# Kernel optimization log

Hardware: AMD Instinct MI355X
Metric: run time of the kernel (lower is better)

## Reference

```python
import jax, jax.numpy as jnp
from jax import lax
import numpy as np

B, T, I, H, C = 32, 256, 128, 128, 100


def setup_inputs() -> dict:
    key = jax.random.key(0)
    ks = jax.random.split(key, 9)
    s = 1.0 / np.sqrt(H)  # PyTorch LSTMCell init range
    inp = {
        "x": jax.random.normal(ks[0], (B, T, I), dtype=jnp.float32),
        "w_ih": jax.random.uniform(ks[1], (4 * H, I), jnp.float32, -s, s),
        "b_ih": jax.random.uniform(ks[2], (4 * H,), jnp.float32, -s, s),
        "w_hh": jax.random.uniform(ks[3], (4 * H, H), jnp.float32, -s, s),
        "b_hh": jax.random.uniform(ks[4], (4 * H,), jnp.float32, -s, s),
        # attention params: normal(mean=0, std=0.01) per the source
        "w1": 0.01 * jax.random.normal(ks[5], (2 * H, H), dtype=jnp.float32),
        "w2": 0.01 * jax.random.normal(ks[6], (H, 1), dtype=jnp.float32),
        "w_fc": jax.random.uniform(ks[7], (C, H), jnp.float32, -s, s),
        "b_fc": jax.random.uniform(ks[8], (C,), jnp.float32, -s, s),
    }
    return inp


def _forward(x, w_ih, b_ih, w_hh, b_hh, w1, w2, w_fc, b_fc):
    Bv, Tv, _ = x.shape
    Hv = w_hh.shape[1]
    h0 = jnp.zeros((Bv, Hv), x.dtype)
    c0 = jnp.zeros((Bv, Hv), x.dtype)
    # memory buffer: slot 0 holds the initial zero hidden state (as in the
    # torch code, h_old starts as h_t=0); slots 1..T filled as we go.
    # Unwritten (future) slots are zero, so their attn contribution
    # attn_w * h_old is exactly zero -> no mask needed, matching the
    # growing-memory semantics of the original loop.
    mem0 = jnp.zeros((Bv, Tv + 1, Hv), x.dtype)
    attn0 = jnp.zeros((Bv, Hv), x.dtype)

    def step(carry, inp):
        h, c, mem, _ = carry
        x_t, i = inp
        # PyTorch LSTMCell: gate order i, f, g, o
        gates = x_t @ w_ih.T + b_ih + h @ w_hh.T + b_hh
        ig, fg, gg, og = jnp.split(gates, 4, axis=-1)
        c = jax.nn.sigmoid(fg) * c + jax.nn.sigmoid(ig) * jnp.tanh(gg)
        h = jax.nn.sigmoid(og) * jnp.tanh(c)
        # additive attention scores over the memory (NO softmax in source)
        h_rep = jnp.broadcast_to(h[:, None, :], mem.shape)  # [B, T+1, H]
        cat = jnp.concatenate([h_rep, mem], axis=-1)        # [B, T+1, 2H]
        s = jnp.tanh(cat @ w1) @ w2                          # [B, T+1, 1]
        attn_c = jnp.sum(s * mem, axis=1)                    # [B, H]
        mem = mem.at[:, i + 1, :].set(h)  # append h_t to memory
        return (h, c, mem, attn_c), None

    xs = (jnp.transpose(x, (1, 0, 2)), jnp.arange(Tv))
    (h, c, mem, attn_c), _ = lax.scan(step, (h0, c0, mem0, attn0), xs)
    return (h + attn_c) @ w_fc.T + b_fc


def reference(x, w_ih, b_ih, w_hh, b_hh, w1, w2, w_fc, b_fc):
    return _forward(x, w_ih, b_ih, w_hh, b_hh, w1, w2, w_fc, b_fc)
```

## Files before the change

### kernel.cpp

```cpp
#include <hip/hip_runtime.h>
#include <hip/hip_bf16.h>


#define Bsz 32
#define Tsz 256
#define Isz 128
#define Hsz 128
#define Csz 100
#define G4H 512

__device__ __forceinline__ float2 pk_fma(float2 a, float2 b, float2 c) {
    float2 d;
    asm("v_pk_fma_f32 %0, %1, %2, %3" : "=v"(d) : "v"(a), "v"(b), "v"(c));
    return d;
}
__device__ __forceinline__ float quad_rsum(float x) {
    int t = __builtin_amdgcn_update_dpp(0, __float_as_int(x), 0xB1, 0xF, 0xF, true);
    x += __int_as_float(t);
    t = __builtin_amdgcn_update_dpp(0, __float_as_int(x), 0x4E, 0xF, 0xF, true);
    x += __int_as_float(t);
    return x;
}
__device__ __forceinline__ float rcpf(float x) { return __builtin_amdgcn_rcpf(x); }
__device__ __forceinline__ float sigm_n(float x) { return rcpf(1.0f + __expf(-x)); }
__device__ __forceinline__ float tanh_n(float x) {
    float ax = fabsf(x);
    float e = __expf(-2.0f * ax);
    float t = (1.0f - e) * rcpf(1.0f + e);
    return copysignf(t, x);
}
__device__ __forceinline__ float sigm(float x) { return rcpf(1.0f + __expf(-x)); }
__device__ __forceinline__ float tanh_s(float x) {
    float ax = fabsf(x);
    float e = __expf(-2.0f * ax);
    float t = (1.0f - e) * rcpf(1.0f + e);
    return copysignf(t, x);
}

__global__ __launch_bounds__(256) void prep_kernel(
    const float* __restrict__ w_ih, const float* __restrict__ b_ih,
    const float* __restrict__ w_hh, const float* __restrict__ b_hh,
    float* __restrict__ wih_t, float* __restrict__ whh_pk, float* __restrict__ bias) {
    int idx = blockIdx.x * blockDim.x + threadIdx.x;
    if (idx < G4H * Isz) {
        int j = idx >> 7;
        int k = idx & 127;
        wih_t[k * G4H + j] = w_ih[idx];

        int j4  = idx & 3;
        int q   = (idx >> 2) & 3;
        int d   = (idx >> 4) & 127;
        int gi  = (idx >> 11) & 3;
        int kk4 = (idx >> 13) & 7;
        whh_pk[idx] = w_hh[(size_t)((gi << 7) + d) * 128 + (q << 5) + (kk4 << 2) + j4];
    }
    if (idx < G4H) bias[idx] = b_ih[idx] + b_hh[idx];
}

#define BM 64
#define BN 64
#define BKt 64
#define LDP 68

__global__ __launch_bounds__(256) void gemm_tn(
    const float* __restrict__ A, const float* __restrict__ Bm,
    const float* __restrict__ bias, float* __restrict__ C,
    int M, int N, int K) {
    __shared__ float As[BKt][LDP];
    __shared__ float Bs[BKt][LDP];
    int tid = threadIdx.x;
    int bm = blockIdx.y * BM;
    int bn = blockIdx.x * BN;
    int tx = tid & 15, ty = tid >> 4;
    float acc[4][4] = {};

    int lr = tid >> 4;
    int lc = (tid & 15) * 4;

    for (int k0 = 0; k0 < K; k0 += BKt) {
        #pragma unroll
        for (int p = 0; p < 4; ++p) {
            int row = p * 16 + lr;
            float4 v = *(const float4*)(A + (size_t)(bm + row) * K + k0 + lc);
            As[lc + 0][row] = v.x;
            As[lc + 1][row] = v.y;
            As[lc + 2][row] = v.z;
            As[lc + 3][row] = v.w;
        }
        #pragma unroll
        for (int p = 0; p < 4; ++p) {
            int kr = p * 16 + lr;
            float4 v = *(const float4*)(Bm + (size_t)(k0 + kr) * N + bn + lc);
            *(float4*)&Bs[kr][lc] = v;
        }
        __syncthreads();
        #pragma unroll
        for (int kk = 0; kk < BKt; ++kk) {
            float4 a = *(const float4*)&As[kk][ty * 4];
            float4 b = *(const float4*)&Bs[kk][tx * 4];
            acc[0][0] = fmaf(a.x, b.x, acc[0][0]);
            acc[0][1] = fmaf(a.x, b.y, acc[0][1]);
            acc[0][2] = fmaf(a.x, b.z, acc[0][2]);
            acc[0][3] = fmaf(a.x, b.w, acc[0][3]);
            acc[1][0] = fmaf(a.y, b.x, acc[1][0]);
            acc[1][1] = fmaf(a.y, b.y, acc[1][1]);
            acc[1][2] = fmaf(a.y, b.z, acc[1][2]);
            acc[1][3] = fmaf(a.y, b.w, acc[1][3]);
            acc[2][0] = fmaf(a.z, b.x, acc[2][0]);
            acc[2][1] = fmaf(a.z, b.y, acc[2][1]);
            acc[2][2] = fmaf(a.z, b.z, acc[2][2]);
            acc[2][3] = fmaf(a.z, b.w, acc[2][3]);
            acc[3][0] = fmaf(a.w, b.x, acc[3][0]);
            acc[3][1] = fmaf(a.w, b.y, acc[3][1]);
            acc[3][2] = fmaf(a.w, b.z, acc[3][2]);
            acc[3][3] = fmaf(a.w, b.w, acc[3][3]);
        }
        __syncthreads();
    }
    float bb[4] = {0.f, 0.f, 0.f, 0.f};
    if (bias) {
        bb[0] = bias[bn + tx * 4 + 0];
        bb[1] = bias[bn + tx * 4 + 1];
        bb[2] = bias[bn + tx * 4 + 2];
        bb[3] = bias[bn + tx * 4 + 3];
    }
    #pragma unroll
    for (int i = 0; i < 4; ++i) {
        int row = bm + ty * 4 + i;
        float4 v;
        v.x = acc[i][0] + bb[0];
        v.y = acc[i][1] + bb[1];
        v.z = acc[i][2] + bb[2];
        v.w = acc[i][3] + bb[3];
        *(float4*)(C + (size_t)row * N + bn + tx * 4) = v;
    }
}

#define HPAD(k) ((k) + 8 * ((k) >> 5))

__global__ __launch_bounds__(512, 2) void lstm_seq(
    const float* __restrict__ G, const float* __restrict__ whh_pk,
    float* __restrict__ H_all) {
    const int b = blockIdx.x;
    const int tid = threadIdx.x;
    const int d = tid >> 2;
    const int q = tid & 3;

    __shared__ float h_s[2][160];

    float2 w2[4][16];
    {
        const float4* wp = (const float4*)whh_pk;
        #pragma unroll
        for (int kk4 = 0; kk4 < 8; ++kk4)
            #pragma unroll
            for (int gi = 0; gi < 4; ++gi) {
                float4 v = wp[((kk4 * 4 + gi) * 128 + d) * 4 + q];
                w2[gi][kk4 * 2]     = make_float2(v.x, v.y);
                w2[gi][kk4 * 2 + 1] = make_float2(v.z, v.w);
            }
    }

    if (tid < 320) ((float*)h_s)[tid] = 0.0f;
    float c = 0.0f;
    __syncthreads();

    const float* Gq = G + (size_t)b * Tsz * G4H + q * 128 + d;
    float* Hb = H_all + (size_t)b * Tsz * Hsz + d;

    float gval = Gq[0];
    int cur = 0;
    for (int t = 0; t < Tsz; ++t) {
        const int tn = (t < Tsz - 1) ? t + 1 : t;
        float ngval = Gq[(size_t)tn * G4H];

        float2 acc0 = make_float2(q == 0 ? gval : 0.f, 0.f);
        float2 acc1 = make_float2(q == 1 ? gval : 0.f, 0.f);
        float2 acc2 = make_float2(q == 2 ? gval : 0.f, 0.f);
        float2 acc3 = make_float2(q == 3 ? gval : 0.f, 0.f);
        const float4* hb4 = (const float4*)&h_s[cur][q * 40];
        #pragma unroll
        for (int kk4 = 0; kk4 < 8; ++kk4) {
            float4 h4 = hb4[kk4];
            float2 hA = make_float2(h4.x, h4.y);
            float2 hB = make_float2(h4.z, h4.w);
            acc0 = pk_fma(hA, w2[0][2 * kk4], acc0);
            acc1 = pk_fma(hA, w2[1][2 * kk4], acc1);
            acc2 = pk_fma(hA, w2[2][2 * kk4], acc2);
            acc3 = pk_fma(hA, w2[3][2 * kk4], acc3);
            acc0 = pk_fma(hB, w2[0][2 * kk4 + 1], acc0);
            acc1 = pk_fma(hB, w2[1][2 * kk4 + 1], acc1);
            acc2 = pk_fma(hB, w2[2][2 * kk4 + 1], acc2);
            acc3 = pk_fma(hB, w2[3][2 * kk4 + 1], acc3);
        }
        float a0 = quad_rsum(acc0.x + acc0.y);
        float a1 = quad_rsum(acc1.x + acc1.y);
        float a2 = quad_rsum(acc2.x + acc2.y);
        float a3 = quad_rsum(acc3.x + acc3.y);

        float iv = sigm_n(a0);
        float fv = sigm_n(a1);
        float gv = tanh_n(a2);
        float ov = sigm_n(a3);
        c = fv * c + iv * gv;
        float h = ov * tanh_n(c);

        int nxt = cur ^ 1;
        if (q == 0) {
            h_s[nxt][HPAD(d)] = h;
            Hb[(size_t)t * Hsz] = h;
        }
        gval = ngval;
        __syncthreads();
        cur = nxt;
    }
}

__global__ __launch_bounds__(256) void attn_out(
    const float* __restrict__ H_all, const float* __restrict__ KV,
    const float* __restrict__ w1, const float* __restrict__ w2,
    const float* __restrict__ w_fc, const float* __restrict__ b_fc,
    float* __restrict__ out) {
    int b = blockIdx.x;
    int tid = threadIdx.x;
    __shared__ float hT[Hsz];
    __shared__ float q_s[Hsz];
    __shared__ float s_s[Tsz];
    __shared__ float r_s[Hsz];

    const float* Hb = H_all + (size_t)b * Tsz * Hsz;
    const float* KVb = KV + (size_t)b * Tsz * Hsz;

    if (tid < Hsz) hT[tid] = Hb[255 * Hsz + tid];
    __syncthreads();
    if (tid < Hsz) {
        float acc = 0.f;
        #pragma unroll 8
        for (int k = 0; k < Hsz; ++k) acc = fmaf(hT[k], w1[k * Hsz + tid], acc);
        q_s[tid] = acc;
    }
    __syncthreads();
    int wave = tid >> 6, lane = tid & 63;
    float w2a = w2[lane], w2b = w2[lane + 64];
    for (int j = wave; j < 255; j += 4) {
        const float* kv = KVb + j * Hsz;
        float v0 = q_s[lane] + kv[lane];
        float v1 = q_s[lane + 64] + kv[lane + 64];
        float p = tanh_s(v0) * w2a + tanh_s(v1) * w2b;
        #pragma unroll
        for (int off = 32; off > 0; off >>= 1) p += __shfl_xor(p, off);
        if (lane == 0) s_s[j] = p;
    }
    __syncthreads();
    if (tid < Hsz) {
        float acc = 0.f;
        #pragma unroll 4
        for (int j = 0; j < 255; ++j) acc = fmaf(s_s[j], Hb[j * Hsz + tid], acc);
        r_s[tid] = hT[tid] + acc;
    }
    __syncthreads();
    if (tid < Csz) {
        float acc = b_fc[tid];
        const float* wr = w_fc + tid * Hsz;
        #pragma unroll 8
        for (int k = 0; k < Hsz; ++k) acc = fmaf(r_s[k], wr[k], acc);
        out[b * Csz + tid] = acc;
    }
}

extern "C" void kernel_launch(void* const* d_in, const int* in_sizes, int n_in,
                              void* d_out, int out_size, void* d_ws, size_t ws_size,
                              hipStream_t stream) {
    const float* x    = (const float*)d_in[0];
    const float* w_ih = (const float*)d_in[1];
    const float* b_ih = (const float*)d_in[2];
    const float* w_hh = (const float*)d_in[3];
    const float* b_hh = (const float*)d_in[4];
    const float* w1   = (const float*)d_in[5];
    const float* w2   = (const float*)d_in[6];
    const float* w_fc = (const float*)d_in[7];
    const float* b_fc = (const float*)d_in[8];

    float* ws = (float*)d_ws;
    float* wih_t  = ws;
    float* whh_pk = wih_t + 65536;
    float* bias   = whh_pk + 65536;
    float* G      = bias + 512;
    float* H_all  = G + 4194304;
    float* KV     = H_all + 1048576;

    prep_kernel<<<256, 256, 0, stream>>>(w_ih, b_ih, w_hh, b_hh, wih_t, whh_pk, bias);

    dim3 g1(G4H / BN, (Bsz * Tsz) / BM);
    gemm_tn<<<g1, 256, 0, stream>>>(x, wih_t, bias, G, Bsz * Tsz, G4H, Isz);

    lstm_seq<<<Bsz, 512, 0, stream>>>(G, whh_pk, H_all);

    dim3 g2(Hsz / BN, (Bsz * Tsz) / BM);
    gemm_tn<<<g2, 256, 0, stream>>>(H_all, w1 + Hsz * Hsz, nullptr, KV, Bsz * Tsz, Hsz, Hsz);

    attn_out<<<Bsz, 256, 0, stream>>>(H_all, KV, w1, w2, w_fc, b_fc, (float*)d_out);
}
```

Measured before the change: 355.5 us.

## Use 128x128 GEMM tiles, batch H stores via ring, and reparallelize attention

```diff
diff --git a/kernel.cpp b/kernel.cpp
--- a/kernel.cpp
+++ b/kernel.cpp
@@ -29,13 +29,7 @@
     float t = (1.0f - e) * rcpf(1.0f + e);
     return copysignf(t, x);
 }
-__device__ __forceinline__ float sigm(float x) { return rcpf(1.0f + __expf(-x)); }
-__device__ __forceinline__ float tanh_s(float x) {
-    float ax = fabsf(x);
-    float e = __expf(-2.0f * ax);
-    float t = (1.0f - e) * rcpf(1.0f + e);
-    return copysignf(t, x);
-}
+__device__ __forceinline__ float tanh_s(float x) { return tanh_n(x); }
 
 __global__ __launch_bounds__(256) void prep_kernel(
     const float* __restrict__ w_ih, const float* __restrict__ b_ih,
@@ -55,6 +49,74 @@
         whh_pk[idx] = w_hh[(size_t)((gi << 7) + d) * 128 + (q << 5) + (kk4 << 2) + j4];
     }
     if (idx < G4H) bias[idx] = b_ih[idx] + b_hh[idx];
+}
+
+#define GBK 16
+#define GLD 132
+
+__global__ __launch_bounds__(256) void gemm128(
+    const float* __restrict__ A, const float* __restrict__ Bm,
+    const float* __restrict__ bias, float* __restrict__ C,
+    int M, int N, int K) {
+    __shared__ float As[GBK][GLD];
+    __shared__ float Bs[GBK][GLD];
+    const int tid = threadIdx.x;
+    const int bm = blockIdx.y * 128;
+    const int bn = blockIdx.x * 128;
+    const int tx = tid & 15, ty = tid >> 4;
+    float acc[8][8] = {};
+
+    const int ar = tid >> 2;
+    const int ac = (tid & 3) * 4;
+    const int br = tid >> 5;
+    const int bc = (tid & 31) * 4;
+
+    for (int k0 = 0; k0 < K; k0 += GBK) {
+        #pragma unroll
+        for (int h = 0; h < 2; ++h) {
+            int r = ar + 64 * h;
+            float4 v = *(const float4*)(A + (size_t)(bm + r) * K + k0 + ac);
+            As[ac + 0][r] = v.x;
+            As[ac + 1][r] = v.y;
+            As[ac + 2][r] = v.z;
+            As[ac + 3][r] = v.w;
+        }
+        #pragma unroll
+        for (int h = 0; h < 2; ++h) {
+            int kr = br + 8 * h;
+            float4 v = *(const float4*)(Bm + (size_t)(k0 + kr) * N + bn + bc);
+            *(float4*)&Bs[kr][bc] = v;
+        }
+        __syncthreads();
+        #pragma unroll
+        for (int kk = 0; kk < GBK; ++kk) {
+            float a[8], b[8];
+            *(float4*)&a[0] = *(const float4*)&As[kk][ty * 8];
+            *(float4*)&a[4] = *(const float4*)&As[kk][ty * 8 + 4];
+            *(float4*)&b[0] = *(const float4*)&Bs[kk][tx * 8];
+            *(float4*)&b[4] = *(const float4*)&Bs[kk][tx * 8 + 4];
+            #pragma unroll
+            for (int i = 0; i < 8; ++i)
+                #pragma unroll
+                for (int j = 0; j < 8; ++j)
+                    acc[i][j] = fmaf(a[i], b[j], acc[i][j]);
+        }
+        __syncthreads();
+    }
+    float bb[8];
+    #pragma unroll
+    for (int j = 0; j < 8; ++j) bb[j] = bias ? bias[bn + tx * 8 + j] : 0.0f;
+    #pragma unroll
+    for (int i = 0; i < 8; ++i) {
+        int row = bm + ty * 8 + i;
+        float4 v0, v1;
+        v0.x = acc[i][0] + bb[0]; v0.y = acc[i][1] + bb[1];
+        v0.z = acc[i][2] + bb[2]; v0.w = acc[i][3] + bb[3];
+        v1.x = acc[i][4] + bb[4]; v1.y = acc[i][5] + bb[5];
+        v1.z = acc[i][6] + bb[6]; v1.w = acc[i][7] + bb[7];
+        *(float4*)(C + (size_t)row * N + bn + tx * 8) = v0;
+        *(float4*)(C + (size_t)row * N + bn + tx * 8 + 4) = v1;
+    }
 }
 
 #define BM 64
@@ -147,8 +209,9 @@
     const int q = tid & 3;
 
     __shared__ float h_s[2][160];
-
-    float2 w2[4][16];
+    __shared__ float ring[8][Hsz];
+
+    float2 w2v[4][16];
     {
         const float4* wp = (const float4*)whh_pk;
         #pragma unroll
@@ -156,8 +219,8 @@
             #pragma unroll
             for (int gi = 0; gi < 4; ++gi) {
                 float4 v = wp[((kk4 * 4 + gi) * 128 + d) * 4 + q];
-                w2[gi][kk4 * 2]     = make_float2(v.x, v.y);
-                w2[gi][kk4 * 2 + 1] = make_float2(v.z, v.w);
+                w2v[gi][kk4 * 2]     = make_float2(v.x, v.y);
+                w2v[gi][kk4 * 2 + 1] = make_float2(v.z, v.w);
             }
     }
 
@@ -166,7 +229,10 @@
     __syncthreads();
 
     const float* Gq = G + (size_t)b * Tsz * G4H + q * 128 + d;
-    float* Hb = H_all + (size_t)b * Tsz * Hsz + d;
+    float* Hb = H_all + (size_t)b * Tsz * Hsz;
+
+    const int fr = tid >> 6;
+    const int fc = (tid * 2) & 127;
 
     float gval = Gq[0];
     int cur = 0;
@@ -174,29 +240,31 @@
         const int tn = (t < Tsz - 1) ? t + 1 : t;
         float ngval = Gq[(size_t)tn * G4H];
 
-        float2 acc0 = make_float2(q == 0 ? gval : 0.f, 0.f);
-        float2 acc1 = make_float2(q == 1 ? gval : 0.f, 0.f);
-        float2 acc2 = make_float2(q == 2 ? gval : 0.f, 0.f);
-        float2 acc3 = make_float2(q == 3 ? gval : 0.f, 0.f);
+        float2 accA[4], accB[4];
+        #pragma unroll
+        for (int gi = 0; gi < 4; ++gi) {
+            accA[gi] = make_float2(q == gi ? gval : 0.f, 0.f);
+            accB[gi] = make_float2(0.f, 0.f);
+        }
         const float4* hb4 = (const float4*)&h_s[cur][q * 40];
         #pragma unroll
         for (int kk4 = 0; kk4 < 8; ++kk4) {
             float4 h4 = hb4[kk4];
             float2 hA = make_float2(h4.x, h4.y);
             float2 hB = make_float2(h4.z, h4.w);
-            acc0 = pk_fma(hA, w2[0][2 * kk4], acc0);
-            acc1 = pk_fma(hA, w2[1][2 * kk4], acc1);
-            acc2 = pk_fma(hA, w2[2][2 * kk4], acc2);
-            acc3 = pk_fma(hA, w2[3][2 * kk4], acc3);
-            acc0 = pk_fma(hB, w2[0][2 * kk4 + 1], acc0);
-            acc1 = pk_fma(hB, w2[1][2 * kk4 + 1], acc1);
-            acc2 = pk_fma(hB, w2[2][2 * kk4 + 1], acc2);
-            acc3 = pk_fma(hB, w2[3][2 * kk4 + 1], acc3);
-        }
-        float a0 = quad_rsum(acc0.x + acc0.y);
-        float a1 = quad_rsum(acc1.x + acc1.y);
-        float a2 = quad_rsum(acc2.x + acc2.y);
-        float a3 = quad_rsum(acc3.x + acc3.y);
+            accA[0] = pk_fma(hA, w2v[0][2 * kk4], accA[0]);
+            accA[1] = pk_fma(hA, w2v[1][2 * kk4], accA[1]);
+            accA[2] = pk_fma(hA, w2v[2][2 * kk4], accA[2]);
+            accA[3] = pk_fma(hA, w2v[3][2 * kk4], accA[3]);
+            accB[0] = pk_fma(hB, w2v[0][2 * kk4 + 1], accB[0]);
+            accB[1] = pk_fma(hB, w2v[1][2 * kk4 + 1], accB[1]);
+            accB[2] = pk_fma(hB, w2v[2][2 * kk4 + 1], accB[2]);
+            accB[3] = pk_fma(hB, w2v[3][2 * kk4 + 1], accB[3]);
+        }
+        float a0 = quad_rsum(accA[0].x + accA[0].y + accB[0].x + accB[0].y);
+        float a1 = quad_rsum(accA[1].x + accA[1].y + accB[1].x + accB[1].y);
+        float a2 = quad_rsum(accA[2].x + accA[2].y + accB[2].x + accB[2].y);
+        float a3 = quad_rsum(accA[3].x + accA[3].y + accB[3].x + accB[3].y);
 
         float iv = sigm_n(a0);
         float fv = sigm_n(a1);
@@ -208,11 +276,16 @@
         int nxt = cur ^ 1;
         if (q == 0) {
             h_s[nxt][HPAD(d)] = h;
-            Hb[(size_t)t * Hsz] = h;
+            ring[t & 7][d] = h;
         }
         gval = ngval;
         __syncthreads();
         cur = nxt;
+
+        if ((t & 7) == 7) {
+            float2 v = *(const float2*)&ring[fr][fc];
+            *(float2*)&Hb[(size_t)(t - 7 + fr) * Hsz + fc] = v;
+        }
     }
 }
 
@@ -225,13 +298,18 @@
     int tid = threadIdx.x;
     __shared__ float hT[Hsz];
     __shared__ float q_s[Hsz];
+    __shared__ float w2s[Hsz];
     __shared__ float s_s[Tsz];
+    __shared__ float r2[2][Hsz];
     __shared__ float r_s[Hsz];
 
     const float* Hb = H_all + (size_t)b * Tsz * Hsz;
     const float* KVb = KV + (size_t)b * Tsz * Hsz;
 
-    if (tid < Hsz) hT[tid] = Hb[255 * Hsz + tid];
+    if (tid < Hsz) {
+        hT[tid] = Hb[255 * Hsz + tid];
+        w2s[tid] = w2[tid];
+    }
     __syncthreads();
     if (tid < Hsz) {
         float acc = 0.f;
@@ -240,31 +318,48 @@
         q_s[tid] = acc;
     }
     __syncthreads();
-    int wave = tid >> 6, lane = tid & 63;
-    float w2a = w2[lane], w2b = w2[lane + 64];
-    for (int j = wave; j < 255; j += 4) {
-        const float* kv = KVb + j * Hsz;
-        float v0 = q_s[lane] + kv[lane];
-        float v1 = q_s[lane + 64] + kv[lane + 64];
-        float p = tanh_s(v0) * w2a + tanh_s(v1) * w2b;
-        #pragma unroll
-        for (int off = 32; off > 0; off >>= 1) p += __shfl_xor(p, off);
-        if (lane == 0) s_s[j] = p;
-    }
-    __syncthreads();
-    if (tid < Hsz) {
+
+    const int qd = tid >> 2, ql = tid & 3;
+    #pragma unroll
+    for (int jj = 0; jj < 4; ++jj) {
+        int j = qd + jj * 64;
+        float p = 0.f;
+        if (j < 255) {
+            const float* kv = KVb + (size_t)j * Hsz + ql * 32;
+            const float* qs = q_s + ql * 32;
+            const float* wv = w2s + ql * 32;
+            #pragma unroll 8
+            for (int k = 0; k < 32; ++k)
+                p = fmaf(tanh_s(qs[k] + kv[k]), wv[k], p);
+        }
+        p = quad_rsum(p);
+        if (ql == 0 && j < 255) s_s[j] = p;
+    }
+    __syncthreads();
+
+    {
+        int dd = tid & 127, half = tid >> 7;
+        int j0 = half * 128, je = half ? 255 : 128;
         float acc = 0.f;
         #pragma unroll 4
-        for (int j = 0; j < 255; ++j) acc = fmaf(s_s[j], Hb[j * Hsz + tid], acc);
-        r_s[tid] = hT[tid] + acc;
-    }
-    __syncthreads();
-    if (tid < Csz) {
-        float acc = b_fc[tid];
-        const float* wr = w_fc + tid * Hsz;
-        #pragma unroll 8
-        for (int k = 0; k < Hsz; ++k) acc = fmaf(r_s[k], wr[k], acc);
-        out[b * Csz + tid] = acc;
+        for (int j = j0; j < je; ++j) acc = fmaf(s_s[j], Hb[(size_t)j * Hsz + dd], acc);
+        r2[half][dd] = acc;
+    }
+    __syncthreads();
+    if (tid < Hsz) r_s[tid] = hT[tid] + r2[0][tid] + r2[1][tid];
+    __syncthreads();
+
+    {
+        int o = tid >> 1, half = tid & 1;
+        float acc = 0.f;
+        if (o < Csz) {
+            const float* wr = w_fc + (size_t)o * Hsz + half * 64;
+            const float* rr = r_s + half * 64;
+            #pragma unroll 8
+            for (int k = 0; k < 64; ++k) acc = fmaf(rr[k], wr[k], acc);
+        }
+        acc += __shfl_xor(acc, 1);
+        if (half == 0 && o < Csz) out[b * Csz + o] = acc + b_fc[o];
     }
 }
 
@@ -291,8 +386,8 @@
 
     prep_kernel<<<256, 256, 0, stream>>>(w_ih, b_ih, w_hh, b_hh, wih_t, whh_pk, bias);
 
-    dim3 g1(G4H / BN, (Bsz * Tsz) / BM);
-    gemm_tn<<<g1, 256, 0, stream>>>(x, wih_t, bias, G, Bsz * Tsz, G4H, Isz);
+    dim3 g1(G4H / 128, (Bsz * Tsz) / 128);
+    gemm128<<<g1, 256, 0, stream>>>(x, wih_t, bias, G, Bsz * Tsz, G4H, Isz);
 
     lstm_seq<<<Bsz, 512, 0, stream>>>(G, whh_pk, H_all);
 
```

Measured after the change: 345.5 us. 2.8% less time.
